# Kernel tuning notes

Measured on AMD Instinct MI355X. Metric: run time of the kernel, lower is better.

Reference implementation:

```python
import jax, jax.numpy as jnp
import numpy as np

TPS = (10.0, 20.0, 30.0)   # Tps init arg (per-segment period)
EPS = 1e-4                 # jitter added to GP predictive covariance
SEG_LEN = 50               # len(ts[j]) for every segment


def setup_inputs() -> dict:
    key = jax.random.key(0)
    k1, k2, k3 = jax.random.split(key, 3)
    K, M, D, T = 16, 128, 16, 302  # T = 2 + 50 + 100 + 150
    z = jax.random.normal(k1, (K, M, D, T), dtype=jnp.float32)
    # sorted time points in (0, Tp_j) per segment, shape [C, SEG_LEN]
    ts = jnp.sort(jax.random.uniform(k2, (3, SEG_LEN), dtype=jnp.float32)
                  * jnp.asarray(TPS, jnp.float32)[:, None], axis=1)
    # log_tau param (D,), tau around tau_init=1.5
    log_tau = jnp.log(1.0 + jax.random.uniform(k3, (16,), dtype=jnp.float32))
    sldj = jnp.zeros((), jnp.float32)
    return {"z": z, "ts": ts, "log_tau": log_tau, "sum_log_det_jacobians": sldj}


def reference(z, ts, log_tau, sum_log_det_jacobians):
    # z: [K,M,D,T]; ts: [C,SEG_LEN]; log_tau: [D]
    tau = jnp.exp(log_tau)                      # [D]
    z_first = z[..., 0:1]                       # [K,M,D,1]
    z_last = z[..., 1:2]                        # [K,M,D,1]
    z_EP = jnp.concatenate([z_first, z_last], axis=-1)  # [K,M,D,2]
    C, seg = ts.shape
    ts_flat = ts.reshape(-1)
    ldj = sum_log_det_jacobians
    t_ind = 2
    outs = []
    for j in range(C):  # C=3 structurally distinct segment sizes
        m = (j + 1) * seg                       # middle_len
        ts_mid = ts_flat[:m]
        ts_j = jnp.concatenate([jnp.array([0.0, TPS[j]], ts.dtype), ts_mid])  # [m+2]
        ds = ts_j[:, None] - ts_j[None, :]      # [m+2,m+2]
        # squared-exp kernel, batched over all D dims at once
        Kmat = jnp.exp(-(ds ** 2)[None] / (2.0 * tau[:, None, None] ** 2))  # [D,n,n]
        K_EPEP_inv = jnp.linalg.inv(Kmat[:, :2, :2])          # [D,2,2]
        K_predEP = Kmat[:, 2:, :2]                            # [D,m,2]
        A_mu = jnp.einsum('dpe,def->dpf', K_predEP, K_EPEP_inv)  # [D,m,2]
        # conditional mean: A_mu @ z_EP  -> [K,M,D,m]
        z_GP_mu = jnp.einsum('dpe,bsde->bsdp', A_mu, z_EP)
        # conditional covariance  K_predpred - K_predEP K_EPEP^{-1} K_EPpred
        Sigma = Kmat[:, 2:, 2:] - jnp.einsum('dpe,dqe->dpq', A_mu, K_predEP)
        Sigma = Sigma + EPS * jnp.eye(m, dtype=Sigma.dtype)
        L = jnp.linalg.cholesky(Sigma)                        # [D,m,m]
        diag = jnp.diagonal(L, axis1=1, axis2=2)              # [D,m]
        # sum_i log|prod(diag_i)| == sum log|diag| (Cholesky diag > 0)
        ldj = ldj + jnp.sum(jnp.log(jnp.abs(diag)))
        z_mid = z[..., t_ind:t_ind + m]                       # [K,M,D,m]
        t_ind += m
        Lz = jnp.einsum('dpq,bsdq->bsdp', L, z_mid)           # [K,M,D,m]
        z_hat = z_GP_mu + Lz
        outs.append(jnp.concatenate([z_first, z_hat, z_last], axis=-1))  # [K,M,D,m+2]
    z_out = jnp.concatenate(outs, axis=-1)  # [K,M,D, sum_j(m_j+2)] = [16,128,16,306]
    return z_out, ldj
```

## Files before the change

kernel.cpp:

```cpp
#include <hip/hip_runtime.h>

#define LB0_OFF 0
#define LB1_OFF 36864
#define LB2_OFF 158720
#define PART_OFF 373760

typedef __attribute__((ext_vector_type(8))) short bf8_t;
typedef __attribute__((ext_vector_type(8))) unsigned short us8_t;
typedef __attribute__((ext_vector_type(4))) float f32x4;

__device__ __forceinline__ int tri_i(int p) { return (p * (p + 1)) >> 1; }

__device__ __forceinline__ void tri_decode(int e, int& r, int& c) {
  r = (int)((sqrtf(8.0f * (float)e + 1.0f) - 1.0f) * 0.5f);
  if (tri_i(r + 1) <= e) ++r;
  if (tri_i(r) > e) --r;
  c = e - tri_i(r);
}

__device__ __forceinline__ unsigned short f2bf(float f) {
  unsigned u = __builtin_bit_cast(unsigned, f);
  u = (u + 0x7FFFu + ((u >> 16) & 1u)) >> 16;
  return (unsigned short)u;
}

__global__ __launch_bounds__(1024) void build_kernel(const float* __restrict__ ts,
                                                     const float* __restrict__ log_tau,
                                                     float* __restrict__ ws)
{
  __shared__ float sS[12880];
  __shared__ __attribute__((aligned(16))) float sU[160 * 20];
  __shared__ __attribute__((aligned(16))) float sW[160 * 20];
  __shared__ float stj[152];
  __shared__ float sAmu[304];
  __shared__ float sKp[304];
  __shared__ float red[1024];

  const int j = blockIdx.x >> 4;
  const int d = blockIdx.x & 15;
  const int m = (j + 1) * 50;
  const int mp    = (j == 0) ? 64      : ((j == 1) ? 112     : 160);
  const int ks    = (j == 0) ? 72      : ((j == 1) ? 136     : 168);
  const int lboff = (j == 0) ? LB0_OFF : ((j == 1) ? LB1_OFF : LB2_OFF);
  const float tpsj = (j == 0) ? 10.0f : ((j == 1) ? 20.0f : 30.0f);
  const int tid  = threadIdx.x;
  const int lane = tid & 63;
  const int wid  = tid >> 6;

  const float tau = expf(log_tau[d]);
  const float cc = 1.0f / (2.0f * tau * tau);

  for (int i = tid; i < m; i += 1024) stj[i] = ts[i];
  __syncthreads();

  const float k01 = expf(-tpsj * tpsj * cc);
  const float det = 1.0f - k01 * k01;
  const float i00 = 1.0f / det;
  const float i01 = -k01 / det;

  for (int p = tid; p < m; p += 1024) {
    float tp = stj[p];
    float kp0 = expf(-tp * tp * cc);
    float dt = tp - tpsj;
    float kp1 = expf(-dt * dt * cc);
    sKp[p * 2 + 0] = kp0; sKp[p * 2 + 1] = kp1;
    sAmu[p * 2 + 0] = fmaf(kp0, i00, kp1 * i01);
    sAmu[p * 2 + 1] = fmaf(kp0, i01, kp1 * i00);
  }
  __syncthreads();

  const int tot = tri_i(mp);
  for (int e = tid; e < tot; e += 1024) {
    int r, q;
    tri_decode(e, r, q);
    float v;
    if (r < m) {
      float dq = stj[r] - stj[q];
      v = expf(-dq * dq * cc)
        - fmaf(sAmu[r * 2], sKp[q * 2], sAmu[r * 2 + 1] * sKp[q * 2 + 1]);
      if (r == q) v += 1e-4f;
    } else {
      v = (r == q) ? 1.0f : 0.0f;
    }
    sS[e] = v;
  }
  __syncthreads();

  const int npan = mp >> 4;
  for (int pb = 0; pb < npan; ++pb) {
    const int kb = pb << 4;
    const int be = kb + 16;

    if (wid == 0) {
      const int tr = lane & 15;
      const int rbase = tri_i(kb + tr) + kb;
      float r[16];
#pragma unroll
      for (int q = 0; q < 16; ++q) r[q] = sS[rbase + q];
#pragma unroll
      for (int kk = 0; kk < 15; ++kk) {
        const float dkk = __shfl(r[kk], kk);
        const float c = r[kk] * (-1.0f / dkk);
#pragma unroll
        for (int q2 = kk + 1; q2 < 16; ++q2) {
          const float cq2 = __shfl(r[kk], q2);
          if (tr > kk && q2 <= tr)
            r[q2] = fmaf(c, cq2, r[q2]);
        }
      }
      if (lane < 16) {
#pragma unroll
        for (int q = 0; q < 16; ++q) if (q <= tr) sS[rbase + q] = r[q];
      }
    }
    __syncthreads();

    if (be < mp) {
      float invd[16];
#pragma unroll
      for (int t = 0; t < 16; ++t)
        invd[t] = 1.0f / sS[tri_i(kb + t) + kb + t];

      {
        const int i = be + tid;
        if (i < mp) {
          const int base = tri_i(i) + kb;
          float r[16];
#pragma unroll
          for (int t = 0; t < 16; ++t) r[t] = sS[base + t];
#pragma unroll
          for (int kk = 0; kk < 15; ++kk) {
            const float c = r[kk] * invd[kk];
#pragma unroll
            for (int q = kk + 1; q < 16; ++q)
              r[q] = fmaf(-c, sS[tri_i(kb + q) + kb + kk], r[q]);
          }
#pragma unroll
          for (int t = 0; t < 16; ++t) sS[base + t] = r[t];
          float w[16];
#pragma unroll
          for (int t = 0; t < 16; ++t) w[t] = r[t] * invd[t];
          float4* up = (float4*)&sU[i * 20];
          float4* wp = (float4*)&sW[i * 20];
#pragma unroll
          for (int c4 = 0; c4 < 4; ++c4) {
            up[c4] = *(float4*)&r[c4 * 4];
            wp[c4] = *(float4*)&w[c4 * 4];
          }
        }
      }
      __syncthreads();

      for (int i0 = be + 4 * wid; i0 < mp; i0 += 64) {
        float wreg[4][16];
        int rb[4];
#pragma unroll
        for (int r = 0; r < 4; ++r) {
          const float4* wp = (const float4*)&sW[(i0 + r) * 20];
#pragma unroll
          for (int c4 = 0; c4 < 4; ++c4)
            *(float4*)&wreg[r][c4 * 4] = wp[c4];
          rb[r] = tri_i(i0 + r);
        }
        for (int q0 = be; q0 <= i0 + 3; q0 += 64) {
          const int q = q0 + lane;
          const int qc = (q <= i0 + 3) ? q : (i0 + 3);
          const float4* up = (const float4*)&sU[qc * 20];
          float u[16];
#pragma unroll
          for (int c4 = 0; c4 < 4; ++c4) *(float4*)&u[c4 * 4] = up[c4];
#pragma unroll
          for (int r = 0; r < 4; ++r) {
            if (q <= i0 + r) {
              const int a = rb[r] + q;
              float acc = sS[a];
#pragma unroll
              for (int t = 0; t < 16; ++t) acc = fmaf(-wreg[r][t], u[t], acc);
              sS[a] = acc;
            }
          }
        }
      }
      __syncthreads();
    }
  }

  float part = 0.0f;
  for (int p = tid; p < m; p += 1024) part += 0.5f * logf(sS[tri_i(p) + p]);
  red[tid] = part;
  __syncthreads();
  for (int s = 512; s > 0; s >>= 1) {
    if (tid < s) red[tid] += red[tid + s];
    __syncthreads();
  }
  if (tid == 0) ws[PART_OFF + blockIdx.x] = red[0];

  unsigned* LBg = (unsigned*)ws + lboff + d * (mp * (ks >> 1));
  const int nwords = mp * (ks >> 1);
  for (int idx = tid; idx < nwords; idx += 1024) {
    const int p = idx / (ks >> 1);
    const int k0 = (idx - p * (ks >> 1)) * 2;
    unsigned short h[2];
#pragma unroll
    for (int e = 0; e < 2; ++e) {
      const int k = k0 + e;
      float v = 0.0f;
      if (p < m) {
        if (k < m) {
          if (k <= p) {
            const float dq = sS[tri_i(k) + k];
            v = (k == p) ? sqrtf(dq) : sS[tri_i(p) + k] * rsqrtf(dq);
          }
        } else if (k == m)     v = sAmu[p * 2 + 0];
        else if (k == m + 1)   v = sAmu[p * 2 + 1];
      }
      h[e] = f2bf(v);
    }
    LBg[idx] = (unsigned)h[0] | ((unsigned)h[1] << 16);
  }
}

template <int M, int MP, int KS, int KT, int TOFF, int OOFF, int LBOFF>
__device__ __forceinline__ void apply_impl(const float* __restrict__ z,
                                           const unsigned* __restrict__ wsu,
                                           float* __restrict__ out,
                                           char* smem, int blk)
{
  constexpr int PT = MP / 16;
  constexpr int PTH = (PT + 1) / 2;
  constexpr int CK = KS / 8;
  const int d   = blk & 15;
  const int bs0 = ((blk >> 4) & 63) * 32;
  const int tid = threadIdx.x;
  const int lane = tid & 63;
  const int wv   = tid >> 6;
  const int rt   = wv & 1;
  const int ph   = wv >> 1;

  unsigned short* Zs = (unsigned short*)smem;

  for (int idx = tid; idx < 32 * CK; idx += 256) {
    const int r = idx / CK;
    const int k0 = (idx - r * CK) * 8;
    const float* zr = z + (size_t)((bs0 + r) * 16 + d) * 302;
    us8_t v;
    if (k0 + 8 <= M) {
#pragma unroll
      for (int t = 0; t < 4; ++t) {
        const float2 f = *(const float2*)(zr + TOFF + k0 + 2 * t);
        v[2 * t]     = f2bf(f.x);
        v[2 * t + 1] = f2bf(f.y);
      }
    } else {
#pragma unroll
      for (int e = 0; e < 8; ++e) {
        const int k = k0 + e;
        float f;
        if (k < M)           f = zr[TOFF + k];
        else if (k == M)     f = zr[0];
        else if (k == M + 1) f = zr[1];
        else                 f = 0.0f;
        v[e] = f2bf(f);
      }
    }
    *(us8_t*)&Zs[r * KS + k0] = v;
  }

  if (tid < 64) {
    const int r = tid >> 1;
    const int which = tid & 1;
    const float* zr = z + (size_t)((bs0 + r) * 16 + d) * 302;
    out[(size_t)((bs0 + r) * 16 + d) * 306 + OOFF + (which ? (M + 1) : 0)] = zr[which];
  }
  __syncthreads();

  bf8_t afr[KT];
  {
    const int row = rt * 16 + (lane & 15);
    const int koff = (lane >> 4) * 8;
#pragma unroll
    for (int kt = 0; kt < KT; ++kt)
      afr[kt] = *(const bf8_t*)&Zs[row * KS + kt * 32 + koff];
  }

  const unsigned short* LBd = (const unsigned short*)(wsu + LBOFF + d * (MP * (KS / 2)));
  const int pt0 = ph * PTH;
  const int pt1 = (ph == 0) ? PTH : PT;
  for (int pt = pt0; pt < pt1; ++pt) {
    const int p = pt * 16 + (lane & 15);
    const unsigned short* bb = &LBd[p * KS + (lane >> 4) * 8];
    f32x4 acc = {0.0f, 0.0f, 0.0f, 0.0f};
#pragma unroll
    for (int kt = 0; kt < KT; ++kt) {
      const bf8_t bfr = *(const bf8_t*)&bb[kt * 32];
      acc = __builtin_amdgcn_mfma_f32_16x16x32_bf16(afr[kt], bfr, acc, 0, 0, 0);
    }
    if (p < M) {
      const int rbase = bs0 + rt * 16 + (lane >> 4) * 4;
#pragma unroll
      for (int e = 0; e < 4; ++e)
        out[(size_t)((rbase + e) * 16 + d) * 306 + OOFF + 1 + p] = acc[e];
    }
  }
}

__global__ __launch_bounds__(256) void apply_kernel(const float* __restrict__ z,
                                                    const unsigned* __restrict__ wsu,
                                                    float* __restrict__ out)
{
  __shared__ __attribute__((aligned(16))) char smem[10752];
  const int bid = blockIdx.x;
  if (bid < 1024)      apply_impl<150, 160, 168, 5, 152, 154, LB2_OFF>(z, wsu, out, smem, bid);
  else if (bid < 2048) apply_impl<100, 112, 136, 4,  52,  52, LB1_OFF>(z, wsu, out, smem, bid - 1024);
  else                 apply_impl< 50,  64,  72, 2,   2,   0, LB0_OFF>(z, wsu, out, smem, bid - 2048);
}

__global__ void finalize_kernel(const float* __restrict__ ws_part,
                                const float* __restrict__ sldj,
                                float* __restrict__ out, int last)
{
  if (threadIdx.x == 0) {
    float s = sldj[0];
    for (int i = 0; i < 48; ++i) s += ws_part[i];
    out[last] = s;
  }
}

extern "C" void kernel_launch(void* const* d_in, const int* in_sizes, int n_in,
                              void* d_out, int out_size, void* d_ws, size_t ws_size,
                              hipStream_t stream)
{
  const float* z       = (const float*)d_in[0];
  const float* ts      = (const float*)d_in[1];
  const float* log_tau = (const float*)d_in[2];
  const float* sldj    = (const float*)d_in[3];
  float* out = (float*)d_out;
  float* ws  = (float*)d_ws;

  hipLaunchKernelGGL(build_kernel, dim3(48), dim3(1024), 0, stream, ts, log_tau, ws);
  hipLaunchKernelGGL(apply_kernel, dim3(3072), dim3(256), 0, stream,
                     z, (const unsigned*)ws, out);
  hipLaunchKernelGGL(finalize_kernel, dim3(1), dim3(64), 0, stream,
                     ws + PART_OFF, sldj, out, out_size - 1);
}
```

Before: 190.3 us.

## Merge Cholesky panel factor and trailing solve into one barrier phase

The build kernel's blocked Cholesky drops to 512 threads. Each wave now factorises the 16x16 diagonal panel redundantly in registers and broadcasts it with readlane, so the panel solve reuses the factor without a separate barrier and LDS round trip. Reciprocals use the hardware rcp instruction, and the block reduction now uses wave shuffles. This cuts the barriers per panel step and the LDS traffic, but adds redundant panel work across waves, gives fewer threads for the trailing update, and makes the reciprocals slightly less precise.

```diff
diff --git a/kernel.cpp b/kernel.cpp
--- a/kernel.cpp
+++ b/kernel.cpp
@@ -24,9 +24,16 @@
   return (unsigned short)u;
 }
 
-__global__ __launch_bounds__(1024) void build_kernel(const float* __restrict__ ts,
-                                                     const float* __restrict__ log_tau,
-                                                     float* __restrict__ ws)
+__device__ __forceinline__ float blane(float v, int l) {
+  return __builtin_bit_cast(float, __builtin_amdgcn_readlane(__builtin_bit_cast(int, v), l));
+}
+__device__ __forceinline__ float fastrcp(float x) { return __builtin_amdgcn_rcpf(x); }
+
+#define BNT 512
+
+__global__ __launch_bounds__(BNT) void build_kernel(const float* __restrict__ ts,
+                                                    const float* __restrict__ log_tau,
+                                                    float* __restrict__ ws)
 {
   __shared__ float sS[12880];
   __shared__ __attribute__((aligned(16))) float sU[160 * 20];
@@ -34,7 +41,7 @@
   __shared__ float stj[152];
   __shared__ float sAmu[304];
   __shared__ float sKp[304];
-  __shared__ float red[1024];
+  __shared__ float red[8];
 
   const int j = blockIdx.x >> 4;
   const int d = blockIdx.x & 15;
@@ -50,7 +57,7 @@
   const float tau = expf(log_tau[d]);
   const float cc = 1.0f / (2.0f * tau * tau);
 
-  for (int i = tid; i < m; i += 1024) stj[i] = ts[i];
+  for (int i = tid; i < m; i += BNT) stj[i] = ts[i];
   __syncthreads();
 
   const float k01 = expf(-tpsj * tpsj * cc);
@@ -58,7 +65,7 @@
   const float i00 = 1.0f / det;
   const float i01 = -k01 / det;
 
-  for (int p = tid; p < m; p += 1024) {
+  for (int p = tid; p < m; p += BNT) {
     float tp = stj[p];
     float kp0 = expf(-tp * tp * cc);
     float dt = tp - tpsj;
@@ -70,7 +77,7 @@
   __syncthreads();
 
   const int tot = tri_i(mp);
-  for (int e = tid; e < tot; e += 1024) {
+  for (int e = tid; e < tot; e += BNT) {
     int r, q;
     tri_decode(e, r, q);
     float v;
@@ -87,71 +94,69 @@
   __syncthreads();
 
   const int npan = mp >> 4;
+  const int tr = lane & 15;
   for (int pb = 0; pb < npan; ++pb) {
     const int kb = pb << 4;
     const int be = kb + 16;
-
-    if (wid == 0) {
-      const int tr = lane & 15;
-      const int rbase = tri_i(kb + tr) + kb;
-      float r[16];
-#pragma unroll
-      for (int q = 0; q < 16; ++q) r[q] = sS[rbase + q];
+    const int rbase = tri_i(kb + tr) + kb;
+
+    float rd[16];
+    float invd[16];
+    if (wid < 3) {
+#pragma unroll
+      for (int q = 0; q < 16; ++q) rd[q] = sS[rbase + q];
 #pragma unroll
       for (int kk = 0; kk < 15; ++kk) {
-        const float dkk = __shfl(r[kk], kk);
-        const float c = r[kk] * (-1.0f / dkk);
+        const float dkk = blane(rd[kk], kk);
+        const float ri = fastrcp(dkk);
+        invd[kk] = ri;
+        const float c = -rd[kk] * ri;
 #pragma unroll
         for (int q2 = kk + 1; q2 < 16; ++q2) {
-          const float cq2 = __shfl(r[kk], q2);
-          if (tr > kk && q2 <= tr)
-            r[q2] = fmaf(c, cq2, r[q2]);
-        }
-      }
-      if (lane < 16) {
-#pragma unroll
-        for (int q = 0; q < 16; ++q) if (q <= tr) sS[rbase + q] = r[q];
+          const float cq2 = blane(rd[kk], q2);
+          if (tr > kk && q2 <= tr) rd[q2] = fmaf(c, cq2, rd[q2]);
+        }
+      }
+      invd[15] = fastrcp(blane(rd[15], 15));
+    }
+
+    if (be < mp) {
+      const int i = be + tid;
+      if (i < mp) {
+        const int base = tri_i(i) + kb;
+        float r[16];
+#pragma unroll
+        for (int t = 0; t < 16; ++t) r[t] = sS[base + t];
+#pragma unroll
+        for (int kk = 0; kk < 15; ++kk) {
+          const float c = r[kk] * invd[kk];
+#pragma unroll
+          for (int q = kk + 1; q < 16; ++q)
+            r[q] = fmaf(-c, blane(rd[kk], q), r[q]);
+        }
+#pragma unroll
+        for (int t = 0; t < 16; ++t) sS[base + t] = r[t];
+        float w[16];
+#pragma unroll
+        for (int t = 0; t < 16; ++t) w[t] = r[t] * invd[t];
+        float4* up = (float4*)&sU[i * 20];
+        float4* wp = (float4*)&sW[i * 20];
+#pragma unroll
+        for (int c4 = 0; c4 < 4; ++c4) {
+          up[c4] = *(float4*)&r[c4 * 4];
+          wp[c4] = *(float4*)&w[c4 * 4];
+        }
       }
     }
     __syncthreads();
 
+    if (wid == 0 && lane < 16) {
+#pragma unroll
+      for (int q = 0; q < 16; ++q) if (q <= tr) sS[rbase + q] = rd[q];
+    }
+
     if (be < mp) {
-      float invd[16];
-#pragma unroll
-      for (int t = 0; t < 16; ++t)
-        invd[t] = 1.0f / sS[tri_i(kb + t) + kb + t];
-
-      {
-        const int i = be + tid;
-        if (i < mp) {
-          const int base = tri_i(i) + kb;
-          float r[16];
-#pragma unroll
-          for (int t = 0; t < 16; ++t) r[t] = sS[base + t];
-#pragma unroll
-          for (int kk = 0; kk < 15; ++kk) {
-            const float c = r[kk] * invd[kk];
-#pragma unroll
-            for (int q = kk + 1; q < 16; ++q)
-              r[q] = fmaf(-c, sS[tri_i(kb + q) + kb + kk], r[q]);
-          }
-#pragma unroll
-          for (int t = 0; t < 16; ++t) sS[base + t] = r[t];
-          float w[16];
-#pragma unroll
-          for (int t = 0; t < 16; ++t) w[t] = r[t] * invd[t];
-          float4* up = (float4*)&sU[i * 20];
-          float4* wp = (float4*)&sW[i * 20];
-#pragma unroll
-          for (int c4 = 0; c4 < 4; ++c4) {
-            up[c4] = *(float4*)&r[c4 * 4];
-            wp[c4] = *(float4*)&w[c4 * 4];
-          }
-        }
-      }
-      __syncthreads();
-
-      for (int i0 = be + 4 * wid; i0 < mp; i0 += 64) {
+      for (int i0 = be + 4 * wid; i0 < mp; i0 += 32) {
         float wreg[4][16];
         int rb[4];
 #pragma unroll
@@ -181,23 +186,26 @@
           }
         }
       }
-      __syncthreads();
-    }
+    }
+    __syncthreads();
   }
 
   float part = 0.0f;
-  for (int p = tid; p < m; p += 1024) part += 0.5f * logf(sS[tri_i(p) + p]);
-  red[tid] = part;
-  __syncthreads();
-  for (int s = 512; s > 0; s >>= 1) {
-    if (tid < s) red[tid] += red[tid + s];
-    __syncthreads();
-  }
-  if (tid == 0) ws[PART_OFF + blockIdx.x] = red[0];
+  for (int p = tid; p < m; p += BNT) part += 0.5f * logf(sS[tri_i(p) + p]);
+#pragma unroll
+  for (int off = 32; off > 0; off >>= 1) part += __shfl_down(part, off);
+  if (lane == 0) red[wid] = part;
+  __syncthreads();
+  if (tid == 0) {
+    float s = 0.0f;
+#pragma unroll
+    for (int w8 = 0; w8 < 8; ++w8) s += red[w8];
+    ws[PART_OFF + blockIdx.x] = s;
+  }
 
   unsigned* LBg = (unsigned*)ws + lboff + d * (mp * (ks >> 1));
   const int nwords = mp * (ks >> 1);
-  for (int idx = tid; idx < nwords; idx += 1024) {
+  for (int idx = tid; idx < nwords; idx += BNT) {
     const int p = idx / (ks >> 1);
     const int k0 = (idx - p * (ks >> 1)) * 2;
     unsigned short h[2];
@@ -337,7 +345,7 @@
   float* out = (float*)d_out;
   float* ws  = (float*)d_ws;
 
-  hipLaunchKernelGGL(build_kernel, dim3(48), dim3(1024), 0, stream, ts, log_tau, ws);
+  hipLaunchKernelGGL(build_kernel, dim3(48), dim3(BNT), 0, stream, ts, log_tau, ws);
   hipLaunchKernelGGL(apply_kernel, dim3(3072), dim3(256), 0, stream,
                      z, (const unsigned*)ws, out);
   hipLaunchKernelGGL(finalize_kernel, dim3(1), dim3(64), 0, stream,
```

Measured after the change: 177.5 us. 1.07x faster.
